# Kernel tuning notes

Hardware: AMD Instinct MI355X
Metric: run time of the kernel (lower is better)

Reference implementation:

```python
import jax, jax.numpy as jnp
import numpy as np

K, d = 8, 8
D = K * d          # 64
B, T, N = 8, 12, 325


def _xavier(key, shape):
    fan_out, fan_in = shape
    lim = (6.0 / (fan_in + fan_out)) ** 0.5
    return jax.random.uniform(key, shape, jnp.float32, -lim, lim)


def setup_inputs() -> dict:
    key = jax.random.key(0)
    ks = jax.random.split(key, 8)
    return {
        "X": jax.random.normal(ks[0], (B, T, N, D), jnp.float32),
        "STE": jax.random.normal(ks[1], (B, T, N, D), jnp.float32),
        "adj": jax.random.randint(ks[2], (N, N), 0, 2, jnp.int32),
        "W7": _xavier(ks[3], (D, 2 * D)), "b7": jnp.zeros((D,), jnp.float32),
        "W8": _xavier(ks[4], (D, 2 * D)), "b8": jnp.zeros((D,), jnp.float32),
        "W9": _xavier(ks[5], (D, 2 * D)), "b9": jnp.zeros((D,), jnp.float32),
        "W10": _xavier(ks[6], (D, D)), "b10": jnp.zeros((D,), jnp.float32),
        "W11": _xavier(ks[7], (D, D)), "b11": jnp.zeros((D,), jnp.float32),
    }


def reference(X, STE, adj, W7, b7, W8, b8, W9, b9, W10, b10, W11, b11):
    # X, STE: [B, T, N, D]
    x = jnp.concatenate([X, STE], axis=-1)  # [B,T,N,2D]
    gelu = lambda t: jax.nn.gelu(t, approximate=False)  # torch F.gelu default = exact erf
    q = gelu(x @ W7.T + b7)  # [B,T,N,D]
    k = gelu(x @ W8.T + b8)
    v = gelu(x @ W9.T + b9)
    # split D into K heads of size d (equivalent to torch split(dim=-1)+cat(dim=0))
    heads = lambda t: t.reshape(B, T, N, K, d)
    q, k, v = heads(q), heads(k), heads(v)
    # scores: [K,B,T,N,N] == torch's [K*B,T,N,N]
    attn = jnp.einsum('btnkd,btmkd->kbtnm', q, k) / (d ** 0.5)
    attn = jnp.where(adj > 0, attn, jnp.float32(-9e15))
    attn = jax.nn.softmax(attn, axis=-1)
    out = jnp.einsum('kbtnm,btmkd->btnkd', attn, v).reshape(B, T, N, D)
    out = gelu(out @ W10.T + b10) @ W11.T + b11
    return out
```

## Files before the change

kernel.cpp:

```cpp
#include <hip/hip_runtime.h>
#include <math.h>

#define NN 325
#define BT 96
#define NROWS (BT * NN)
#define SCL (0.35355339059327373f * 1.4426950408889634f)
#define QKV_BLKS ((NROWS + 63) / 64)
#define PREP_ITEMS (11 * NN + 8192)
#define PREP_BLKS ((PREP_ITEMS + 511) / 512)
#define TOT_BLKS (QKV_BLKS + PREP_BLKS)
#define HSTR (NN * 8)

typedef _Float16 half_t;
typedef half_t half8_t __attribute__((ext_vector_type(8)));
typedef half_t half4_t __attribute__((ext_vector_type(4)));
typedef half_t half2_t __attribute__((ext_vector_type(2)));
typedef float float4_t __attribute__((ext_vector_type(4)));

__device__ __forceinline__ float gelu_f(float x) {
    const float z  = 0.70710678118654752f * x;
    const float az = __builtin_fabsf(z);
    const float t  = __builtin_amdgcn_rcpf(__builtin_fmaf(0.3275911f, az, 1.0f));
    float p = __builtin_fmaf(1.061405429f, t, -1.453152027f);
    p = __builtin_fmaf(p, t, 1.421413741f);
    p = __builtin_fmaf(p, t, -0.284496736f);
    p = __builtin_fmaf(p, t, 0.254829592f);
    p *= t;
    const float e = __builtin_amdgcn_exp2f(-az * az * 1.4426950408889634f);
    float er = __builtin_fmaf(-p, e, 1.0f);
    er = __builtin_copysignf(er, z);
    return 0.5f * x * (1.0f + er);
}

#define XS 136
#define PS 72

__device__ __forceinline__ void qkv_stage_wf(const float* __restrict__ src,
                                             half_t* dst, int tid)
{
    #pragma unroll
    for (int idx = tid; idx < 1024; idx += 512) {
        int c = idx >> 4, g = idx & 15;
        const float4* s4 = (const float4*)&src[c * 128 + g * 8];
        float4 a = s4[0], b = s4[1];
        half8_t h;
        h[0] = (half_t)a.x; h[1] = (half_t)a.y;
        h[2] = (half_t)a.z; h[3] = (half_t)a.w;
        h[4] = (half_t)b.x; h[5] = (half_t)b.y;
        h[6] = (half_t)b.z; h[7] = (half_t)b.w;
        *(half8_t*)&dst[c * XS + g * 8] = h;
    }
}

__device__ __forceinline__ void qkv_compute(
    const half_t* x16, const half_t* wb, const float* __restrict__ b,
    half_t* __restrict__ outp, float oscale,
    int row0, int rbase, int ch, int l15, int quad)
{
    float4_t acc[2];
    #pragma unroll
    for (int cc = 0; cc < 2; ++cc) {
        float bias = b[(ch * 2 + cc) * 16 + l15];
        acc[cc] = (float4_t){bias, bias, bias, bias};
    }
    #pragma unroll
    for (int kk = 0; kk < 8; ++kk) {
        half4_t a = *(const half4_t*)&x16[(rbase + l15) * XS + kk * 16 + quad * 4];
        #pragma unroll
        for (int cc = 0; cc < 2; ++cc) {
            half4_t bf = *(const half4_t*)
                &wb[((ch * 2 + cc) * 16 + l15) * XS + kk * 16 + quad * 4];
            acc[cc] = __builtin_amdgcn_mfma_f32_16x16x16f16(a, bf, acc[cc], 0, 0, 0);
        }
    }
    #pragma unroll
    for (int rr = 0; rr < 4; ++rr) {
        int R = row0 + rbase + quad * 4 + rr;
        if (R < NROWS) {
            int bt = R / NN, n = R - bt * NN;
            #pragma unroll
            for (int cc = 0; cc < 2; ++cc) {
                int col = (ch * 2 + cc) * 16 + l15;
                outp[(long)((bt << 3) + (col >> 3)) * HSTR + n * 8 + (col & 7)] =
                    (half_t)(gelu_f(acc[cc][rr]) * oscale);
            }
        }
    }
}

__global__ __launch_bounds__(512) void qkv_kernel(
    const float* __restrict__ X, const float* __restrict__ STE,
    const int* __restrict__ adj,
    const float* __restrict__ W7, const float* __restrict__ b7,
    const float* __restrict__ W8, const float* __restrict__ b8,
    const float* __restrict__ W9, const float* __restrict__ b9,
    const float* __restrict__ W10, const float* __restrict__ W11,
    half_t* __restrict__ q, half_t* __restrict__ k, half_t* __restrict__ v,
    unsigned int* __restrict__ packedT, half_t* __restrict__ wab)
{
    const int tid = threadIdx.x;
    const int bx  = blockIdx.x;

    if (bx >= QKV_BLKS) {
        int idx = (bx - QKV_BLKS) * 512 + tid;
        if (idx < 11 * NN) {
            int w = idx / NN, n = idx - w * NN;
            unsigned int bits = 0u;
            #pragma unroll 8
            for (int j = 0; j < 32; ++j) {
                int m = w * 32 + j;
                if (m < NN && adj[n * NN + m] > 0) bits |= (1u << j);
            }
            packedT[w * NN + n] = bits;
        } else if (idx < PREP_ITEMS) {
            int i = idx - 11 * NN;
            int p = i >> 12, r = i & 4095;
            wab[i] = (half_t)(p ? W11[r] : W10[r]);
        }
        return;
    }

    __shared__ __attribute__((aligned(16))) half_t x16[64 * XS];
    __shared__ __attribute__((aligned(16))) half_t wbuf[2][64 * XS];
    const int row0 = bx * 64;

    #pragma unroll
    for (int idx = tid; idx < 2048; idx += 512) {
        int r = idx >> 5, c4 = idx & 31;
        int R = row0 + r;
        float4 f = {0.f, 0.f, 0.f, 0.f};
        if (R < NROWS)
            f = (c4 < 16) ? *(const float4*)(X + R * 64 + c4 * 4)
                          : *(const float4*)(STE + R * 64 + (c4 - 16) * 4);
        half4_t hv;
        hv[0] = (half_t)f.x; hv[1] = (half_t)f.y;
        hv[2] = (half_t)f.z; hv[3] = (half_t)f.w;
        *(half4_t*)&x16[r * XS + c4 * 4] = hv;
    }
    qkv_stage_wf(W7, wbuf[0], tid);
    __syncthreads();

    const int lane = tid & 63, wv = tid >> 6;
    const int l15 = lane & 15, quad = lane >> 4;
    const int rbase = (wv & 3) * 16, ch = wv >> 2;

    qkv_stage_wf(W8, wbuf[1], tid);
    qkv_compute(x16, wbuf[0], b7, q, SCL, row0, rbase, ch, l15, quad);
    __syncthreads();

    qkv_stage_wf(W9, wbuf[0], tid);
    qkv_compute(x16, wbuf[1], b8, k, 1.0f, row0, rbase, ch, l15, quad);
    __syncthreads();

    qkv_compute(x16, wbuf[0], b9, v, 1.0f, row0, rbase, ch, l15, quad);
}

__global__ __launch_bounds__(512) void attn_kernel(
    const half_t* __restrict__ q16g, const half_t* __restrict__ k16g,
    const half_t* __restrict__ v16g, const unsigned int* __restrict__ packedT,
    half_t* __restrict__ ao)
{
    __shared__ __attribute__((aligned(16))) half_t K16[336 * 20];
    __shared__ __attribute__((aligned(16))) half_t VT16[16 * 344];
    __shared__ float smax8[8];
    const int tid = threadIdx.x;
    const int bx  = blockIdx.x;
    const int h   = bx / BT;
    const int bt  = bx - h * BT;
    const long qbase = (long)((bt << 3) + h) * HSTR;
    const long baseO = (long)(bt * NN) * 64 + h * 8;

    const half4_t z4 = {(half_t)0.f, (half_t)0.f, (half_t)0.f, (half_t)0.f};

    for (int idx = tid; idx < 16 * 344 / 2; idx += 512)
        if (idx < 1376 || idx >= 1548)
            ((half2_t*)VT16)[idx] = (half2_t)(half_t)0.f;
    for (int i = tid; i < 344; i += 512)
        VT16[8 * 344 + i] = (half_t)1.0f;

    float nk2 = 0.0f;
    for (int r = tid; r < 336; r += 512) {
        half4_t ka = z4, kbv = z4;
        if (r < NN) {
            ka  = *(const half4_t*)(k16g + qbase + r * 8);
            kbv = *(const half4_t*)(k16g + qbase + r * 8 + 4);
        }
        *(half4_t*)&K16[r * 20]      = ka;
        *(half4_t*)&K16[r * 20 + 4]  = kbv;
        *(half4_t*)&K16[r * 20 + 8]  = z4;
        *(half4_t*)&K16[r * 20 + 12] = z4;
        #pragma unroll
        for (int j = 0; j < 4; ++j) {
            float fa = (float)ka[j], fb = (float)kbv[j];
            nk2 = fmaf(fa, fa, nk2);
            nk2 = fmaf(fb, fb, nk2);
        }
    }

    for (int mp = tid; mp < 168; mp += 512) {
        int m0 = 2 * mp, m1 = 2 * mp + 1;
        half4_t v0a = z4, v0b = z4, v1a = z4, v1b = z4;
        if (m0 < NN) {
            v0a = *(const half4_t*)(v16g + qbase + m0 * 8);
            v0b = *(const half4_t*)(v16g + qbase + m0 * 8 + 4);
        }
        if (m1 < NN) {
            v1a = *(const half4_t*)(v16g + qbase + m1 * 8);
            v1b = *(const half4_t*)(v16g + qbase + m1 * 8 + 4);
        }
        #pragma unroll
        for (int c = 0; c < 4; ++c) {
            half2_t p0; p0[0] = v0a[c]; p0[1] = v1a[c];
            half2_t p1; p1[0] = v0b[c]; p1[1] = v1b[c];
            *(half2_t*)&VT16[c * 344 + 2 * mp]       = p0;
            *(half2_t*)&VT16[(c + 4) * 344 + 2 * mp] = p1;
        }
    }

    #pragma unroll
    for (int off = 32; off >= 1; off >>= 1)
        nk2 = fmaxf(nk2, __shfl_xor(nk2, off, 64));
    if ((tid & 63) == 0) smax8[tid >> 6] = nk2;
    __syncthreads();

    const float maxk2 = fmaxf(
        fmaxf(fmaxf(smax8[0], smax8[1]), fmaxf(smax8[2], smax8[3])),
        fmaxf(fmaxf(smax8[4], smax8[5]), fmaxf(smax8[6], smax8[7])));

    const int lane = tid & 63;
    const int wv   = tid >> 6;
    const int l15  = lane & 15;
    const int quad = lane >> 4;
    const int qsh  = quad * 4;

    for (int t = wv; t < 21; t += 8) {
        const int n  = t * 16 + l15;
        const int nq = (n < NN) ? n : (NN - 1);

        half4_t qf = z4;
        if (quad < 2)
            qf = *(const half4_t*)(q16g + qbase + (long)nq * 8 + qsh);

        float ssq = 0.0f;
        #pragma unroll
        for (int j = 0; j < 4; ++j) {
            float fq = (float)qf[j];
            ssq = fmaf(fq, fq, ssq);
        }
        ssq += __shfl_xor(ssq, 16, 64);
        ssq += __shfl_xor(ssq, 32, 64);
        const float rm = sqrtf(ssq * maxk2);

        unsigned int mb[11];
        #pragma unroll
        for (int w = 0; w < 11; ++w) mb[w] = packedT[w * NN + nq];

        const float4_t cinit = {-rm, -rm, -rm, -rm};
        float4_t acc = {0.f, 0.f, 0.f, 0.f};
        #pragma unroll
        for (int mt = 0; mt < 21; ++mt) {
            half4_t kf = *(const half4_t*)&K16[(mt * 16 + l15) * 20 + qsh];
            float4_t sv = __builtin_amdgcn_mfma_f32_16x16x16f16(
                kf, qf, cinit, 0, 0, 0);
            unsigned int sh = mb[mt >> 1] >> (((mt & 1) << 4) + qsh);
            float p0 = (sh & 1u) ? __builtin_amdgcn_exp2f(sv[0]) : 0.f;
            float p1 = (sh & 2u) ? __builtin_amdgcn_exp2f(sv[1]) : 0.f;
            float p2 = (sh & 4u) ? __builtin_amdgcn_exp2f(sv[2]) : 0.f;
            float p3 = (sh & 8u) ? __builtin_amdgcn_exp2f(sv[3]) : 0.f;
            half4_t pf;
            pf[0] = (half_t)p0; pf[1] = (half_t)p1;
            pf[2] = (half_t)p2; pf[3] = (half_t)p3;
            half4_t vf = *(const half4_t*)&VT16[l15 * 344 + mt * 16 + qsh];
            acc = __builtin_amdgcn_mfma_f32_16x16x16f16(vf, pf, acc, 0, 0, 0);
        }

        float sum = __shfl(acc[0], 32 + l15, 64);

        if (quad < 2 && n < NN) {
            float inv = 1.0f / sum;
            half4_t o;
            o[0] = (half_t)(acc[0] * inv); o[1] = (half_t)(acc[1] * inv);
            o[2] = (half_t)(acc[2] * inv); o[3] = (half_t)(acc[3] * inv);
            *(half4_t*)(ao + baseO + (long)n * 64 + qsh) = o;
        }
    }
}

__global__ __launch_bounds__(512) void proj_kernel(
    const half_t* __restrict__ ao, const half_t* __restrict__ wab,
    const float* __restrict__ b10, const float* __restrict__ b11,
    float* __restrict__ out)
{
    __shared__ __attribute__((aligned(16))) half_t a16[64 * PS];
    __shared__ __attribute__((aligned(16))) half_t wA[64 * PS];
    __shared__ __attribute__((aligned(16))) half_t wB[64 * PS];
    __shared__ __attribute__((aligned(16))) half_t h16[64 * PS];
    const int tid  = threadIdx.x;
    const int row0 = blockIdx.x * 64;

    for (int idx = tid; idx < 512; idx += 512) {
        int r = idx >> 3, c8 = idx & 7;
        int R = row0 + r;
        uint4 u = {0u, 0u, 0u, 0u};
        if (R < NROWS) u = *(const uint4*)(ao + (long)R * 64 + c8 * 8);
        *(uint4*)&a16[r * PS + c8 * 8] = u;
        *(uint4*)&wA[r * PS + c8 * 8] = *(const uint4*)&wab[r * 64 + c8 * 8];
        *(uint4*)&wB[r * PS + c8 * 8] = *(const uint4*)&wab[4096 + r * 64 + c8 * 8];
    }
    __syncthreads();

    const int lane = tid & 63, wv = tid >> 6;
    const int l15 = lane & 15, quad = lane >> 4;
    const int rbase = (wv & 3) * 16, ch = wv >> 2;

    float4_t acc[2];
    #pragma unroll
    for (int cc = 0; cc < 2; ++cc) {
        float bias = b10[(ch * 2 + cc) * 16 + l15];
        acc[cc] = (float4_t){bias, bias, bias, bias};
    }
    #pragma unroll
    for (int kk = 0; kk < 4; ++kk) {
        half4_t a = *(const half4_t*)&a16[(rbase + l15) * PS + kk * 16 + quad * 4];
        #pragma unroll
        for (int cc = 0; cc < 2; ++cc) {
            half4_t bf = *(const half4_t*)
                &wA[((ch * 2 + cc) * 16 + l15) * PS + kk * 16 + quad * 4];
            acc[cc] = __builtin_amdgcn_mfma_f32_16x16x16f16(a, bf, acc[cc], 0, 0, 0);
        }
    }
    #pragma unroll
    for (int cc = 0; cc < 2; ++cc) {
        #pragma unroll
        for (int rr = 0; rr < 4; ++rr)
            h16[(rbase + quad * 4 + rr) * PS + (ch * 2 + cc) * 16 + l15] =
                (half_t)gelu_f(acc[cc][rr]);
    }
    __syncthreads();

    #pragma unroll
    for (int cc = 0; cc < 2; ++cc) {
        float bias = b11[(ch * 2 + cc) * 16 + l15];
        acc[cc] = (float4_t){bias, bias, bias, bias};
    }
    #pragma unroll
    for (int kk = 0; kk < 4; ++kk) {
        half4_t a = *(const half4_t*)&h16[(rbase + l15) * PS + kk * 16 + quad * 4];
        #pragma unroll
        for (int cc = 0; cc < 2; ++cc) {
            half4_t bf = *(const half4_t*)
                &wB[((ch * 2 + cc) * 16 + l15) * PS + kk * 16 + quad * 4];
            acc[cc] = __builtin_amdgcn_mfma_f32_16x16x16f16(a, bf, acc[cc], 0, 0, 0);
        }
    }
    #pragma unroll
    for (int cc = 0; cc < 2; ++cc) {
        #pragma unroll
        for (int rr = 0; rr < 4; ++rr) {
            int R = row0 + rbase + quad * 4 + rr;
            if (R < NROWS)
                out[R * 64 + (ch * 2 + cc) * 16 + l15] = acc[cc][rr];
        }
    }
}

extern "C" void kernel_launch(void* const* d_in, const int* in_sizes, int n_in,
                              void* d_out, int out_size, void* d_ws, size_t ws_size,
                              hipStream_t stream) {
    const float* X   = (const float*)d_in[0];
    const float* STE = (const float*)d_in[1];
    const int*   adj = (const int*)d_in[2];
    const float* W7  = (const float*)d_in[3];
    const float* b7  = (const float*)d_in[4];
    const float* W8  = (const float*)d_in[5];
    const float* b8  = (const float*)d_in[6];
    const float* W9  = (const float*)d_in[7];
    const float* b9  = (const float*)d_in[8];
    const float* W10 = (const float*)d_in[9];
    const float* b10 = (const float*)d_in[10];
    const float* W11 = (const float*)d_in[11];
    const float* b11 = (const float*)d_in[12];

    char* wsb = (char*)d_ws;
    const long S = (long)NROWS * 64;
    half_t* qb = (half_t*)wsb;
    half_t* kb = qb + S;
    half_t* vb = qb + 2 * S;
    half_t* ab = qb + 3 * S;
    unsigned int* pk = (unsigned int*)(wsb + 4 * S * sizeof(half_t));
    half_t* wab = (half_t*)(wsb + 4 * S * sizeof(half_t) + 16384);

    qkv_kernel<<<dim3(TOT_BLKS), 512, 0, stream>>>(
        X, STE, adj, W7, b7, W8, b8, W9, b9, W10, W11,
        qb, kb, vb, pk, wab);
    attn_kernel<<<dim3(8 * BT), 512, 0, stream>>>(qb, kb, vb, pk, ab);
    proj_kernel<<<dim3((NROWS + 63) / 64), 512, 0, stream>>>(
        ab, wab, b10, b11, (float*)d_out);
}
```

Baseline: 139.9 us.

## Fuse projection into attention kernel via last-block-done atomic counter

Merges the output projection kernel into the attention kernel. Each of the 8 head blocks for a (b,t) slice bumps an atomic counter, and the last one to finish runs the two-layer MLP projection over all 325 rows of that slice, reusing shared memory through a union. The qkv prep blocks zero the counters. This removes one kernel launch and its inter-kernel gap, at the cost of serialising the projection onto 96 tail blocks and adding fences and atomics.

```diff
diff --git a/kernel.cpp b/kernel.cpp
--- a/kernel.cpp
+++ b/kernel.cpp
@@ -6,7 +6,7 @@
 #define NROWS (BT * NN)
 #define SCL (0.35355339059327373f * 1.4426950408889634f)
 #define QKV_BLKS ((NROWS + 63) / 64)
-#define PREP_ITEMS (11 * NN + 8192)
+#define PREP_ITEMS (11 * NN + 8192 + 96)
 #define PREP_BLKS ((PREP_ITEMS + 511) / 512)
 #define TOT_BLKS (QKV_BLKS + PREP_BLKS)
 #define HSTR (NN * 8)
@@ -96,7 +96,8 @@
     const float* __restrict__ W9, const float* __restrict__ b9,
     const float* __restrict__ W10, const float* __restrict__ W11,
     half_t* __restrict__ q, half_t* __restrict__ k, half_t* __restrict__ v,
-    unsigned int* __restrict__ packedT, half_t* __restrict__ wab)
+    unsigned int* __restrict__ packedT, half_t* __restrict__ wab,
+    int* __restrict__ cnt)
 {
     const int tid = threadIdx.x;
     const int bx  = blockIdx.x;
@@ -112,10 +113,12 @@
                 if (m < NN && adj[n * NN + m] > 0) bits |= (1u << j);
             }
             packedT[w * NN + n] = bits;
-        } else if (idx < PREP_ITEMS) {
+        } else if (idx < 11 * NN + 8192) {
             int i = idx - 11 * NN;
             int p = i >> 12, r = i & 4095;
             wab[i] = (half_t)(p ? W11[r] : W10[r]);
+        } else if (idx < PREP_ITEMS) {
+            cnt[idx - (11 * NN + 8192)] = 0;
         }
         return;
     }
@@ -155,14 +158,25 @@
     qkv_compute(x16, wbuf[0], b9, v, 1.0f, row0, rbase, ch, l15, quad);
 }
 
-__global__ __launch_bounds__(512) void attn_kernel(
+union __attribute__((aligned(16))) SMAttn {
+    struct { half_t K16[336 * 20]; half_t VT16[16 * 344]; } a;
+    struct { half_t a16[64 * PS]; half_t wA[64 * PS];
+             half_t wB[64 * PS];  half_t h16[64 * PS]; } p;
+};
+
+__global__ __launch_bounds__(512) void attnproj_kernel(
     const half_t* __restrict__ q16g, const half_t* __restrict__ k16g,
     const half_t* __restrict__ v16g, const unsigned int* __restrict__ packedT,
-    half_t* __restrict__ ao)
+    const half_t* __restrict__ wab,
+    const float* __restrict__ b10, const float* __restrict__ b11,
+    half_t* __restrict__ ao, float* __restrict__ out, int* __restrict__ cnt)
 {
-    __shared__ __attribute__((aligned(16))) half_t K16[336 * 20];
-    __shared__ __attribute__((aligned(16))) half_t VT16[16 * 344];
+    __shared__ SMAttn sm;
     __shared__ float smax8[8];
+    __shared__ int srank;
+    half_t* K16  = sm.a.K16;
+    half_t* VT16 = sm.a.VT16;
+
     const int tid = threadIdx.x;
     const int bx  = blockIdx.x;
     const int h   = bx / BT;
@@ -284,82 +298,95 @@
             *(half4_t*)(ao + baseO + (long)n * 64 + qsh) = o;
         }
     }
-}
-
-__global__ __launch_bounds__(512) void proj_kernel(
-    const half_t* __restrict__ ao, const half_t* __restrict__ wab,
-    const float* __restrict__ b10, const float* __restrict__ b11,
-    float* __restrict__ out)
-{
-    __shared__ __attribute__((aligned(16))) half_t a16[64 * PS];
-    __shared__ __attribute__((aligned(16))) half_t wA[64 * PS];
-    __shared__ __attribute__((aligned(16))) half_t wB[64 * PS];
-    __shared__ __attribute__((aligned(16))) half_t h16[64 * PS];
-    const int tid  = threadIdx.x;
-    const int row0 = blockIdx.x * 64;
+
+    __syncthreads();
+    __threadfence();
+    __syncthreads();
+    if (tid == 0) srank = atomicAdd(&cnt[bt], 1);
+    __syncthreads();
+    if (srank != 7) return;
+
+    __threadfence();
+
+    half_t* a16 = sm.p.a16;
+    half_t* wA  = sm.p.wA;
+    half_t* wB  = sm.p.wB;
+    half_t* h16 = sm.p.h16;
 
     for (int idx = tid; idx < 512; idx += 512) {
         int r = idx >> 3, c8 = idx & 7;
-        int R = row0 + r;
-        uint4 u = {0u, 0u, 0u, 0u};
-        if (R < NROWS) u = *(const uint4*)(ao + (long)R * 64 + c8 * 8);
-        *(uint4*)&a16[r * PS + c8 * 8] = u;
         *(uint4*)&wA[r * PS + c8 * 8] = *(const uint4*)&wab[r * 64 + c8 * 8];
         *(uint4*)&wB[r * PS + c8 * 8] = *(const uint4*)&wab[4096 + r * 64 + c8 * 8];
     }
-    __syncthreads();
-
-    const int lane = tid & 63, wv = tid >> 6;
-    const int l15 = lane & 15, quad = lane >> 4;
+
     const int rbase = (wv & 3) * 16, ch = wv >> 2;
 
-    float4_t acc[2];
-    #pragma unroll
-    for (int cc = 0; cc < 2; ++cc) {
-        float bias = b10[(ch * 2 + cc) * 16 + l15];
-        acc[cc] = (float4_t){bias, bias, bias, bias};
-    }
-    #pragma unroll
-    for (int kk = 0; kk < 4; ++kk) {
-        half4_t a = *(const half4_t*)&a16[(rbase + l15) * PS + kk * 16 + quad * 4];
+    for (int t64 = 0; t64 < 6; ++t64) {
+        const int row0 = bt * NN + t64 * 64;
+        const int vr   = (t64 == 5) ? (NN - 5 * 64) : 64;
+        __syncthreads();
+
+        for (int idx = tid; idx < 512; idx += 512) {
+            int r = idx >> 3, c8 = idx & 7;
+            uint4 u = {0u, 0u, 0u, 0u};
+            if (r < vr) u = *(const uint4*)(ao + (long)(row0 + r) * 64 + c8 * 8);
+            *(uint4*)&a16[r * PS + c8 * 8] = u;
+        }
+        __syncthreads();
+
+        float4_t acc2[2];
         #pragma unroll
         for (int cc = 0; cc < 2; ++cc) {
-            half4_t bf = *(const half4_t*)
-                &wA[((ch * 2 + cc) * 16 + l15) * PS + kk * 16 + quad * 4];
-            acc[cc] = __builtin_amdgcn_mfma_f32_16x16x16f16(a, bf, acc[cc], 0, 0, 0);
-        }
-    }
-    #pragma unroll
-    for (int cc = 0; cc < 2; ++cc) {
-        #pragma unroll
-        for (int rr = 0; rr < 4; ++rr)
-            h16[(rbase + quad * 4 + rr) * PS + (ch * 2 + cc) * 16 + l15] =
-                (half_t)gelu_f(acc[cc][rr]);
-    }
-    __syncthreads();
-
-    #pragma unroll
-    for (int cc = 0; cc < 2; ++cc) {
-        float bias = b11[(ch * 2 + cc) * 16 + l15];
-        acc[cc] = (float4_t){bias, bias, bias, bias};
-    }
-    #pragma unroll
-    for (int kk = 0; kk < 4; ++kk) {
-        half4_t a = *(const half4_t*)&h16[(rbase + l15) * PS + kk * 16 + quad * 4];
+            float bias = b10[(ch * 2 + cc) * 16 + l15];
+            acc2[cc] = (float4_t){bias, bias, bias, bias};
+        }
+        #pragma unroll
+        for (int kk = 0; kk < 4; ++kk) {
+            half4_t a = *(const half4_t*)
+                &a16[(rbase + l15) * PS + kk * 16 + quad * 4];
+            #pragma unroll
+            for (int cc = 0; cc < 2; ++cc) {
+                half4_t bf = *(const half4_t*)
+                    &wA[((ch * 2 + cc) * 16 + l15) * PS + kk * 16 + quad * 4];
+                acc2[cc] = __builtin_amdgcn_mfma_f32_16x16x16f16(
+                    a, bf, acc2[cc], 0, 0, 0);
+            }
+        }
         #pragma unroll
         for (int cc = 0; cc < 2; ++cc) {
-            half4_t bf = *(const half4_t*)
-                &wB[((ch * 2 + cc) * 16 + l15) * PS + kk * 16 + quad * 4];
-            acc[cc] = __builtin_amdgcn_mfma_f32_16x16x16f16(a, bf, acc[cc], 0, 0, 0);
-        }
-    }
-    #pragma unroll
-    for (int cc = 0; cc < 2; ++cc) {
-        #pragma unroll
-        for (int rr = 0; rr < 4; ++rr) {
-            int R = row0 + rbase + quad * 4 + rr;
-            if (R < NROWS)
-                out[R * 64 + (ch * 2 + cc) * 16 + l15] = acc[cc][rr];
+            #pragma unroll
+            for (int rr = 0; rr < 4; ++rr)
+                h16[(rbase + quad * 4 + rr) * PS + (ch * 2 + cc) * 16 + l15] =
+                    (half_t)gelu_f(acc2[cc][rr]);
+        }
+        __syncthreads();
+
+        #pragma unroll
+        for (int cc = 0; cc < 2; ++cc) {
+            float bias = b11[(ch * 2 + cc) * 16 + l15];
+            acc2[cc] = (float4_t){bias, bias, bias, bias};
+        }
+        #pragma unroll
+        for (int kk = 0; kk < 4; ++kk) {
+            half4_t a = *(const half4_t*)
+                &h16[(rbase + l15) * PS + kk * 16 + quad * 4];
+            #pragma unroll
+            for (int cc = 0; cc < 2; ++cc) {
+                half4_t bf = *(const half4_t*)
+                    &wB[((ch * 2 + cc) * 16 + l15) * PS + kk * 16 + quad * 4];
+                acc2[cc] = __builtin_amdgcn_mfma_f32_16x16x16f16(
+                    a, bf, acc2[cc], 0, 0, 0);
+            }
+        }
+        #pragma unroll
+        for (int cc = 0; cc < 2; ++cc) {
+            #pragma unroll
+            for (int rr = 0; rr < 4; ++rr) {
+                int rloc = rbase + quad * 4 + rr;
+                if (rloc < vr)
+                    out[(long)(row0 + rloc) * 64 + (ch * 2 + cc) * 16 + l15] =
+                        acc2[cc][rr];
+            }
         }
     }
 }
@@ -389,11 +416,11 @@
     half_t* ab = qb + 3 * S;
     unsigned int* pk = (unsigned int*)(wsb + 4 * S * sizeof(half_t));
     half_t* wab = (half_t*)(wsb + 4 * S * sizeof(half_t) + 16384);
+    int* cnt = (int*)(wab + 8192);
 
     qkv_kernel<<<dim3(TOT_BLKS), 512, 0, stream>>>(
         X, STE, adj, W7, b7, W8, b8, W9, b9, W10, W11,
-        qb, kb, vb, pk, wab);
-    attn_kernel<<<dim3(8 * BT), 512, 0, stream>>>(qb, kb, vb, pk, ab);
-    proj_kernel<<<dim3((NROWS + 63) / 64), 512, 0, stream>>>(
-        ab, wab, b10, b11, (float*)d_out);
-}
+        qb, kb, vb, pk, wab, cnt);
+    attnproj_kernel<<<dim3(8 * BT), 512, 0, stream>>>(
+        qb, kb, vb, pk, wab, b10, b11, ab, (float*)d_out, cnt);
+}
```

After: 255.1 us. +82.4%, slower.
